# Optimization experiments

Measured on AMD Instinct MI355X. Metric: run time of the kernel, lower is better.

The kernel has to match this reference:

```python
import jax, jax.numpy as jnp
import numpy as np

DIM, N_HEAD, DK, DV = 1024, 16, 64, 64
B, S = 1, 4096


def setup_inputs() -> dict:
    key = jax.random.key(0)
    ks = jax.random.split(key, 9)
    sd = 0.02
    return {
        "x": jax.random.normal(ks[0], (B, S, DIM), dtype=jnp.float32),
        "Wq": jax.random.normal(ks[1], (DIM, N_HEAD * DK), dtype=jnp.float32) * sd,
        "bq": jnp.zeros((N_HEAD * DK,), dtype=jnp.float32),
        "Wk": jax.random.normal(ks[2], (DIM, N_HEAD * DK), dtype=jnp.float32) * sd,
        "bk": jnp.zeros((N_HEAD * DK,), dtype=jnp.float32),
        "Wv": jax.random.normal(ks[3], (DIM, N_HEAD * DV), dtype=jnp.float32) * sd,
        "bv": jnp.zeros((N_HEAD * DV,), dtype=jnp.float32),
        "Wo": jax.random.normal(ks[4], (N_HEAD * DV, DIM), dtype=jnp.float32) * sd,
        "bo": jnp.zeros((DIM,), dtype=jnp.float32),
    }


def reference(x, Wq, bq, Wk, bk, Wv, bv, Wo, bo):
    b, s, _ = x.shape
    scale = DK ** (-0.5)
    # projections -> [b, h, s, d]
    q = (x @ Wq + bq).reshape(b, s, N_HEAD, DK).transpose(0, 2, 1, 3)
    k = (x @ Wk + bk).reshape(b, s, N_HEAD, DK).transpose(0, 2, 1, 3)
    v = (x @ Wv + bv).reshape(b, s, N_HEAD, DV).transpose(0, 2, 1, 3)
    attn = jnp.einsum("bhqd,bhkd->bhqk", q, k) * scale  # [b,h,s,s]
    attn = jax.nn.softmax(attn, axis=-1)
    out = jnp.einsum("bhqk,bhkd->bhqd", attn, v)  # [b,h,s,dv]
    out = out.transpose(0, 2, 1, 3).reshape(b, s, N_HEAD * DV)
    return out @ Wo + bo
```

## Files before the change

kernel.cpp:

```cpp
#include <hip/hip_runtime.h>
#include <hip/hip_bf16.h>
#include <hip/hip_fp16.h>

#define SEQ 4096
#define DIM 1024
#define NH 16

typedef __attribute__((ext_vector_type(4))) float f32x4;
typedef __attribute__((ext_vector_type(8))) _Float16 half8;
typedef __attribute__((ext_vector_type(4))) _Float16 half4;

#if __has_builtin(__builtin_amdgcn_exp2f)
#define EXP2(x) __builtin_amdgcn_exp2f(x)
#else
#define EXP2(x) exp2f(x)
#endif


__global__ __launch_bounds__(256) void conv_x(const float* __restrict__ x,
                                              _Float16* __restrict__ xh, int n) {
  int i = (blockIdx.x * 256 + threadIdx.x) * 4;
  if (i >= n) return;
  float4 v = *reinterpret_cast<const float4*>(x + i);
  half4 h;
  h[0] = (_Float16)v.x; h[1] = (_Float16)v.y;
  h[2] = (_Float16)v.z; h[3] = (_Float16)v.w;
  *reinterpret_cast<half4*>(xh + i) = h;
}

__global__ __launch_bounds__(256) void conv_wT4(const float* __restrict__ W0,
                                                const float* __restrict__ W1,
                                                const float* __restrict__ W2,
                                                const float* __restrict__ W3,
                                                _Float16* __restrict__ T0,
                                                _Float16* __restrict__ T1,
                                                _Float16* __restrict__ T2,
                                                _Float16* __restrict__ T3) {
  const float* W = blockIdx.z == 0 ? W0 : blockIdx.z == 1 ? W1 : blockIdx.z == 2 ? W2 : W3;
  _Float16* Wt = blockIdx.z == 0 ? T0 : blockIdx.z == 1 ? T1 : blockIdx.z == 2 ? T2 : T3;
  __shared__ float t[32][33];
  int bx = blockIdx.x * 32;
  int by = blockIdx.y * 32;
  int tx = threadIdx.x & 31, ty = threadIdx.x >> 5;
#pragma unroll
  for (int i = 0; i < 4; i++)
    t[ty + i * 8][tx] = W[(by + ty + i * 8) * DIM + bx + tx];
  __syncthreads();
#pragma unroll
  for (int i = 0; i < 4; i++)
    Wt[(bx + ty + i * 8) * DIM + by + tx] = (_Float16)t[tx][ty + i * 8];
}

template <int MODE>
__device__ __forceinline__ void gemm_body(const _Float16* __restrict__ A,
                                          const _Float16* __restrict__ Bt,
                                          const float* __restrict__ bias,
                                          void* __restrict__ outp,
                                          int M, int N, int Kd, int bmb, int bnb) {
  __shared__ __align__(16) _Float16 As[64][72];
  __shared__ __align__(16) _Float16 Bs[128][72];
  const int tid = threadIdx.x, lane = tid & 63, w = tid >> 6;
  const int bm = bmb * 64, bn = bnb * 128;
  const int l15 = lane & 15, g = lane >> 4, kb = g * 8;
  const int sra = tid >> 2, sca = (tid & 3) * 16;
  const int srb = tid >> 1, scb = (tid & 1) * 32;
  f32x4 acc[4][2] = {};

  uint4 ar0, ar1, br0, br1, br2, br3;
  auto LOADT = [&](int k0) {
    const _Float16* ap = A + (size_t)(bm + sra) * Kd + k0 + sca;
    ar0 = *reinterpret_cast<const uint4*>(ap);
    ar1 = *reinterpret_cast<const uint4*>(ap + 8);
    const _Float16* bp = Bt + (size_t)(bn + srb) * Kd + k0 + scb;
    br0 = *reinterpret_cast<const uint4*>(bp);
    br1 = *reinterpret_cast<const uint4*>(bp + 8);
    br2 = *reinterpret_cast<const uint4*>(bp + 16);
    br3 = *reinterpret_cast<const uint4*>(bp + 24);
  };

  LOADT(0);
  for (int k0 = 0; k0 < Kd; k0 += 64) {
    __syncthreads();
    *reinterpret_cast<uint4*>(&As[sra][sca]) = ar0;
    *reinterpret_cast<uint4*>(&As[sra][sca + 8]) = ar1;
    *reinterpret_cast<uint4*>(&Bs[srb][scb]) = br0;
    *reinterpret_cast<uint4*>(&Bs[srb][scb + 8]) = br1;
    *reinterpret_cast<uint4*>(&Bs[srb][scb + 16]) = br2;
    *reinterpret_cast<uint4*>(&Bs[srb][scb + 24]) = br3;
    __syncthreads();
    if (k0 + 64 < Kd) LOADT(k0 + 64);
#pragma unroll
    for (int kk = 0; kk < 64; kk += 32) {
      half8 af[4], bf[2];
#pragma unroll
      for (int i = 0; i < 4; i++)
        af[i] = *reinterpret_cast<const half8*>(&As[i * 16 + l15][kk + kb]);
#pragma unroll
      for (int j = 0; j < 2; j++)
        bf[j] = *reinterpret_cast<const half8*>(&Bs[w * 32 + j * 16 + l15][kk + kb]);
      __builtin_amdgcn_s_setprio(1);
#pragma unroll
      for (int i = 0; i < 4; i++)
#pragma unroll
        for (int j = 0; j < 2; j++)
          acc[i][j] = __builtin_amdgcn_mfma_f32_16x16x32_f16(af[i], bf[j], acc[i][j], 0, 0, 0);
      __builtin_amdgcn_s_setprio(0);
    }
  }

#pragma unroll
  for (int i = 0; i < 4; i++)
#pragma unroll
    for (int j = 0; j < 2; j++) {
      const int row0 = bm + i * 16 + g * 4;
      const int col = bn + w * 32 + j * 16 + l15;
      if (MODE == 2) {
        half4 hv;
#pragma unroll
        for (int r = 0; r < 4; r++) hv[r] = (_Float16)(acc[i][j][r] + bias[col]);
        *reinterpret_cast<half4*>(&((_Float16*)outp)[(size_t)col * M + row0]) = hv;
      } else {
#pragma unroll
        for (int r = 0; r < 4; r++) {
          float vv = acc[i][j][r] + bias[col];
          if (MODE == 0) {
            _Float16* O = (_Float16*)outp;
            O[(((col >> 6) * SEQ) + row0 + r) * 64 + (col & 63)] = (_Float16)vv;
          } else {
            float* O = (float*)outp;
            O[(size_t)(row0 + r) * N + col] = vv;
          }
        }
      }
    }
}

__global__ __launch_bounds__(256) void gemm_qkv(const _Float16* __restrict__ A,
                                                const _Float16* __restrict__ WqT,
                                                const _Float16* __restrict__ WkT,
                                                const _Float16* __restrict__ WvT,
                                                const float* __restrict__ bq,
                                                const float* __restrict__ bk,
                                                const float* __restrict__ bv,
                                                _Float16* __restrict__ Qd,
                                                _Float16* __restrict__ Kd,
                                                _Float16* __restrict__ Vd) {
  if (blockIdx.z == 0)
    gemm_body<0>(A, WqT, bq, (void*)Qd, SEQ, DIM, DIM, blockIdx.x, blockIdx.y);
  else if (blockIdx.z == 1)
    gemm_body<0>(A, WkT, bk, (void*)Kd, SEQ, DIM, DIM, blockIdx.x, blockIdx.y);
  else
    gemm_body<2>(A, WvT, bv, (void*)Vd, SEQ, DIM, DIM, blockIdx.x, blockIdx.y);
}

__global__ __launch_bounds__(256) void gemm_out(const _Float16* __restrict__ A,
                                                const _Float16* __restrict__ Bt,
                                                const float* __restrict__ bias,
                                                float* __restrict__ out) {
  gemm_body<1>(A, Bt, bias, (void*)out, SEQ, DIM, DIM, blockIdx.x, blockIdx.y);
}

__global__ __launch_bounds__(256) void attn_fwd(const _Float16* __restrict__ Q,
                                                const _Float16* __restrict__ Kh,
                                                const _Float16* __restrict__ Vt_g,
                                                _Float16* __restrict__ Og) {
  __shared__ __align__(16) _Float16 Ks[64][72];
  __shared__ __align__(16) _Float16 Vs[64][72];
  __shared__ __align__(16) _Float16 Ps[4][2][16][72];
  const int h = blockIdx.y;
  const int q0 = blockIdx.x * 128;
  const int tid = threadIdx.x, lane = tid & 63, w = tid >> 6;
  const int l15 = lane & 15, g = lane >> 4, kb = g * 8;

  const float C = 0.18033688f;

  const int qrow = q0 + w * 32 + l15;
  const _Float16* qp = Q + ((size_t)h * SEQ + qrow) * 64;
  half8 qf[2][2];
  qf[0][0] = *reinterpret_cast<const half8*>(qp + kb);
  qf[0][1] = *reinterpret_cast<const half8*>(qp + 32 + kb);
  qf[1][0] = *reinterpret_cast<const half8*>(qp + 16 * 64 + kb);
  qf[1][1] = *reinterpret_cast<const half8*>(qp + 16 * 64 + 32 + kb);

  f32x4 o[2][4] = {};
  float m[2] = {-1e30f, -1e30f};
  float lsum[2] = {0.f, 0.f};
  float negmC[2] = {1e30f, 1e30f};

  const int srow = tid >> 3, sc8 = (tid & 7) * 8;
  const _Float16* kbase = Kh + (size_t)h * SEQ * 64;
  const _Float16* vbase = Vt_g + (size_t)h * 64 * SEQ;

  uint4 kr0, kr1, vr0, vr1;
  auto LOADKV = [&](int kt2) {
    const _Float16* kp = kbase + (size_t)(kt2 * 64 + srow) * 64 + sc8;
    kr0 = *reinterpret_cast<const uint4*>(kp);
    kr1 = *reinterpret_cast<const uint4*>(kp + 32 * 64);
    const _Float16* vp = vbase + (size_t)srow * SEQ + kt2 * 64 + sc8;
    vr0 = *reinterpret_cast<const uint4*>(vp);
    vr1 = *reinterpret_cast<const uint4*>(vp + 32 * SEQ);
  };

  LOADKV(0);
  for (int kt = 0; kt < SEQ / 64; ++kt) {
    __syncthreads();
    *reinterpret_cast<uint4*>(&Ks[srow][sc8]) = kr0;
    *reinterpret_cast<uint4*>(&Ks[srow + 32][sc8]) = kr1;
    *reinterpret_cast<uint4*>(&Vs[srow][sc8]) = vr0;
    *reinterpret_cast<uint4*>(&Vs[srow + 32][sc8]) = vr1;
    __syncthreads();
    if (kt + 1 < SEQ / 64) LOADKV(kt + 1);

    f32x4 sf[2][4] = {};
    __builtin_amdgcn_s_setprio(1);
#pragma unroll
    for (int f = 0; f < 4; f++) {
      half8 kf0 = *reinterpret_cast<const half8*>(&Ks[f * 16 + l15][kb]);
      half8 kf1 = *reinterpret_cast<const half8*>(&Ks[f * 16 + l15][32 + kb]);
      sf[0][f] = __builtin_amdgcn_mfma_f32_16x16x32_f16(kf0, qf[0][0], sf[0][f], 0, 0, 0);
      sf[0][f] = __builtin_amdgcn_mfma_f32_16x16x32_f16(kf1, qf[0][1], sf[0][f], 0, 0, 0);
      sf[1][f] = __builtin_amdgcn_mfma_f32_16x16x32_f16(kf0, qf[1][0], sf[1][f], 0, 0, 0);
      sf[1][f] = __builtin_amdgcn_mfma_f32_16x16x32_f16(kf1, qf[1][1], sf[1][f], 0, 0, 0);
    }
    __builtin_amdgcn_s_setprio(0);

#pragma unroll
    for (int s = 0; s < 2; s++) {
      float pm = fmaxf(fmaxf(fmaxf(sf[s][0][0], sf[s][0][1]), fmaxf(sf[s][0][2], sf[s][0][3])),
                       fmaxf(fmaxf(sf[s][1][0], sf[s][1][1]), fmaxf(sf[s][1][2], sf[s][1][3])));
      pm = fmaxf(pm, fmaxf(fmaxf(fmaxf(sf[s][2][0], sf[s][2][1]), fmaxf(sf[s][2][2], sf[s][2][3])),
                           fmaxf(fmaxf(sf[s][3][0], sf[s][3][1]), fmaxf(sf[s][3][2], sf[s][3][3]))));
      if (__any(pm > m[s] + 64.f)) {
        pm = fmaxf(pm, __shfl_xor(pm, 16, 64));
        pm = fmaxf(pm, __shfl_xor(pm, 32, 64));
        float mn = fmaxf(m[s], pm);
        float al = EXP2((m[s] - mn) * C);
        m[s] = mn;
        negmC[s] = -mn * C;
        lsum[s] *= al;
#pragma unroll
        for (int f = 0; f < 4; f++) o[s][f] *= al;
      }
      half4 ph[4];
#pragma unroll
      for (int f = 0; f < 4; f++)
#pragma unroll
        for (int r = 0; r < 4; r++) {
          float p = EXP2(fmaf(sf[s][f][r], C, negmC[s]));
          lsum[s] += p;
          ph[f][r] = (_Float16)p;
        }
#pragma unroll
      for (int f = 0; f < 4; f++)
        *reinterpret_cast<half4*>(&Ps[w][s][l15][f * 16 + g * 4]) = ph[f];
    }

    half8 pa[2][2];
#pragma unroll
    for (int s = 0; s < 2; s++) {
      pa[s][0] = *reinterpret_cast<const half8*>(&Ps[w][s][l15][kb]);
      pa[s][1] = *reinterpret_cast<const half8*>(&Ps[w][s][l15][32 + kb]);
    }

    __builtin_amdgcn_s_setprio(1);
#pragma unroll
    for (int f = 0; f < 4; f++) {
      half8 vf0 = *reinterpret_cast<const half8*>(&Vs[f * 16 + l15][kb]);
      half8 vf1 = *reinterpret_cast<const half8*>(&Vs[f * 16 + l15][32 + kb]);
      o[0][f] = __builtin_amdgcn_mfma_f32_16x16x32_f16(vf0, pa[0][0], o[0][f], 0, 0, 0);
      o[0][f] = __builtin_amdgcn_mfma_f32_16x16x32_f16(vf1, pa[0][1], o[0][f], 0, 0, 0);
      o[1][f] = __builtin_amdgcn_mfma_f32_16x16x32_f16(vf0, pa[1][0], o[1][f], 0, 0, 0);
      o[1][f] = __builtin_amdgcn_mfma_f32_16x16x32_f16(vf1, pa[1][1], o[1][f], 0, 0, 0);
    }
    __builtin_amdgcn_s_setprio(0);
  }

#pragma unroll
  for (int s = 0; s < 2; s++) {
    float ls = lsum[s];
    ls += __shfl_xor(ls, 16, 64);
    ls += __shfl_xor(ls, 32, 64);
    float rinv = 1.f / ls;
#pragma unroll
    for (int f = 0; f < 4; f++) {
      half4 hv;
#pragma unroll
      for (int r = 0; r < 4; r++) hv[r] = (_Float16)(o[s][f][r] * rinv);
      *reinterpret_cast<half4*>(
          &Og[(size_t)(qrow + 16 * s) * DIM + h * 64 + f * 16 + g * 4]) = hv;
    }
  }
}


extern "C" void kernel_launch(void* const* d_in, const int* in_sizes, int n_in,
                              void* d_out, int out_size, void* d_ws, size_t ws_size,
                              hipStream_t stream) {
  const float* x  = (const float*)d_in[0];
  const float* Wq = (const float*)d_in[1];
  const float* bq = (const float*)d_in[2];
  const float* Wk = (const float*)d_in[3];
  const float* bk = (const float*)d_in[4];
  const float* Wv = (const float*)d_in[5];
  const float* bv = (const float*)d_in[6];
  const float* Wo = (const float*)d_in[7];
  const float* bo = (const float*)d_in[8];

  char* ws = (char*)d_ws;
  _Float16* xh  = (_Float16*)ws;
  _Float16* WqT = (_Float16*)(ws + (size_t)SEQ * DIM * 2);
  _Float16* WkT = WqT + DIM * DIM;
  _Float16* WvT = WkT + DIM * DIM;
  _Float16* WoT = WvT + DIM * DIM;
  _Float16* Qd  = WoT + DIM * DIM;
  _Float16* Kd  = Qd + (size_t)SEQ * DIM;
  _Float16* Vd  = Kd + (size_t)SEQ * DIM;
  _Float16* Od  = Vd + (size_t)SEQ * DIM;

  conv_x<<<(SEQ * DIM) / 1024, 256, 0, stream>>>(x, xh, SEQ * DIM);
  conv_wT4<<<dim3(32, 32, 4), 256, 0, stream>>>(Wq, Wk, Wv, Wo, WqT, WkT, WvT, WoT);

  gemm_qkv<<<dim3(SEQ / 64, DIM / 128, 3), 256, 0, stream>>>(
      xh, WqT, WkT, WvT, bq, bk, bv, Qd, Kd, Vd);

  attn_fwd<<<dim3(SEQ / 128, NH), 256, 0, stream>>>(Qd, Kd, Vd, Od);

  gemm_out<<<dim3(SEQ / 64, DIM / 128), 256, 0, stream>>>(Od, WoT, bo, (float*)d_out);
}
```

Before: 181.8 us.

## Split attention KV range across two partitions and merge partial softmax results

Splits the key/value sequence of the attention kernel into two partitions along a new grid dimension. Each partition writes unnormalized fp32 partial outputs plus the running max and sum, and a new merge kernel rescales and combines them into the fp16 output. This doubles the number of attention blocks to improve GPU fill and load balance. It costs extra global memory traffic for the fp32 partials, an additional kernel launch, and a larger workspace.

```diff
diff --git a/kernel.cpp b/kernel.cpp
--- a/kernel.cpp
+++ b/kernel.cpp
@@ -5,6 +5,8 @@
 #define SEQ 4096
 #define DIM 1024
 #define NH 16
+#define NSPLIT 2
+#define TILES_PER_PART (SEQ / 64 / NSPLIT)
 
 typedef __attribute__((ext_vector_type(4))) float f32x4;
 typedef __attribute__((ext_vector_type(8))) _Float16 half8;
@@ -15,6 +17,8 @@
 #else
 #define EXP2(x) exp2f(x)
 #endif
+
+#define SMC 0.18033688f
 
 
 __global__ __launch_bounds__(256) void conv_x(const float* __restrict__ x,
@@ -163,16 +167,16 @@
 __global__ __launch_bounds__(256) void attn_fwd(const _Float16* __restrict__ Q,
                                                 const _Float16* __restrict__ Kh,
                                                 const _Float16* __restrict__ Vt_g,
-                                                _Float16* __restrict__ Og) {
+                                                float* __restrict__ Op,
+                                                float2* __restrict__ Ml) {
   __shared__ __align__(16) _Float16 Ks[64][72];
   __shared__ __align__(16) _Float16 Vs[64][72];
   __shared__ __align__(16) _Float16 Ps[4][2][16][72];
   const int h = blockIdx.y;
+  const int part = blockIdx.z;
   const int q0 = blockIdx.x * 128;
   const int tid = threadIdx.x, lane = tid & 63, w = tid >> 6;
   const int l15 = lane & 15, g = lane >> 4, kb = g * 8;
-
-  const float C = 0.18033688f;
 
   const int qrow = q0 + w * 32 + l15;
   const _Float16* qp = Q + ((size_t)h * SEQ + qrow) * 64;
@@ -201,15 +205,16 @@
     vr1 = *reinterpret_cast<const uint4*>(vp + 32 * SEQ);
   };
 
-  LOADKV(0);
-  for (int kt = 0; kt < SEQ / 64; ++kt) {
+  const int t0 = part * TILES_PER_PART, t1 = t0 + TILES_PER_PART;
+  LOADKV(t0);
+  for (int kt = t0; kt < t1; ++kt) {
     __syncthreads();
     *reinterpret_cast<uint4*>(&Ks[srow][sc8]) = kr0;
     *reinterpret_cast<uint4*>(&Ks[srow + 32][sc8]) = kr1;
     *reinterpret_cast<uint4*>(&Vs[srow][sc8]) = vr0;
     *reinterpret_cast<uint4*>(&Vs[srow + 32][sc8]) = vr1;
     __syncthreads();
-    if (kt + 1 < SEQ / 64) LOADKV(kt + 1);
+    if (kt + 1 < t1) LOADKV(kt + 1);
 
     f32x4 sf[2][4] = {};
     __builtin_amdgcn_s_setprio(1);
@@ -234,9 +239,9 @@
         pm = fmaxf(pm, __shfl_xor(pm, 16, 64));
         pm = fmaxf(pm, __shfl_xor(pm, 32, 64));
         float mn = fmaxf(m[s], pm);
-        float al = EXP2((m[s] - mn) * C);
+        float al = EXP2((m[s] - mn) * SMC);
         m[s] = mn;
-        negmC[s] = -mn * C;
+        negmC[s] = -mn * SMC;
         lsum[s] *= al;
 #pragma unroll
         for (int f = 0; f < 4; f++) o[s][f] *= al;
@@ -246,7 +251,7 @@
       for (int f = 0; f < 4; f++)
 #pragma unroll
         for (int r = 0; r < 4; r++) {
-          float p = EXP2(fmaf(sf[s][f][r], C, negmC[s]));
+          float p = EXP2(fmaf(sf[s][f][r], SMC, negmC[s]));
           lsum[s] += p;
           ph[f][r] = (_Float16)p;
         }
@@ -275,21 +280,45 @@
     __builtin_amdgcn_s_setprio(0);
   }
 
+  const size_t prow = ((size_t)part * NH + h) * SEQ;
 #pragma unroll
   for (int s = 0; s < 2; s++) {
     float ls = lsum[s];
     ls += __shfl_xor(ls, 16, 64);
     ls += __shfl_xor(ls, 32, 64);
-    float rinv = 1.f / ls;
+    const size_t rbase = (prow + qrow + 16 * s) * 64;
 #pragma unroll
     for (int f = 0; f < 4; f++) {
-      half4 hv;
-#pragma unroll
-      for (int r = 0; r < 4; r++) hv[r] = (_Float16)(o[s][f][r] * rinv);
-      *reinterpret_cast<half4*>(
-          &Og[(size_t)(qrow + 16 * s) * DIM + h * 64 + f * 16 + g * 4]) = hv;
-    }
+      float4 ov;
+      ov.x = o[s][f][0]; ov.y = o[s][f][1]; ov.z = o[s][f][2]; ov.w = o[s][f][3];
+      *reinterpret_cast<float4*>(&Op[rbase + f * 16 + g * 4]) = ov;
+    }
+    if (g == 0) Ml[prow + qrow + 16 * s] = make_float2(m[s], ls);
   }
+}
+
+__global__ __launch_bounds__(256) void attn_merge(const float* __restrict__ Op,
+                                                  const float2* __restrict__ Ml,
+                                                  _Float16* __restrict__ Og) {
+  const int gid = blockIdx.x * 256 + threadIdx.x;
+  const int dv4 = (gid & 15) * 4;
+  const int row = gid >> 4;
+  const int h = row >> 12, s = row & (SEQ - 1);
+  float2 a = Ml[row];
+  float2 b = Ml[(size_t)NH * SEQ + row];
+  float mm = fmaxf(a.x, b.x);
+  float e1 = EXP2((a.x - mm) * SMC);
+  float e2 = EXP2((b.x - mm) * SMC);
+  float rinv = 1.f / (a.y * e1 + b.y * e2);
+  e1 *= rinv; e2 *= rinv;
+  float4 o1 = *reinterpret_cast<const float4*>(&Op[(size_t)row * 64 + dv4]);
+  float4 o2 = *reinterpret_cast<const float4*>(&Op[((size_t)NH * SEQ + row) * 64 + dv4]);
+  half4 hv;
+  hv[0] = (_Float16)(o1.x * e1 + o2.x * e2);
+  hv[1] = (_Float16)(o1.y * e1 + o2.y * e2);
+  hv[2] = (_Float16)(o1.z * e1 + o2.z * e2);
+  hv[3] = (_Float16)(o1.w * e1 + o2.w * e2);
+  *reinterpret_cast<half4*>(&Og[(size_t)s * DIM + h * 64 + dv4]) = hv;
 }
 
 
@@ -316,6 +345,8 @@
   _Float16* Kd  = Qd + (size_t)SEQ * DIM;
   _Float16* Vd  = Kd + (size_t)SEQ * DIM;
   _Float16* Od  = Vd + (size_t)SEQ * DIM;
+  float*    Opart = (float*)(Od + (size_t)SEQ * DIM);
+  float2*   Mlp   = (float2*)(Opart + (size_t)NSPLIT * NH * SEQ * 64);
 
   conv_x<<<(SEQ * DIM) / 1024, 256, 0, stream>>>(x, xh, SEQ * DIM);
   conv_wT4<<<dim3(32, 32, 4), 256, 0, stream>>>(Wq, Wk, Wv, Wo, WqT, WkT, WvT, WoT);
@@ -323,7 +354,8 @@
   gemm_qkv<<<dim3(SEQ / 64, DIM / 128, 3), 256, 0, stream>>>(
       xh, WqT, WkT, WvT, bq, bk, bv, Qd, Kd, Vd);
 
-  attn_fwd<<<dim3(SEQ / 128, NH), 256, 0, stream>>>(Qd, Kd, Vd, Od);
+  attn_fwd<<<dim3(SEQ / 128, NH, NSPLIT), 256, 0, stream>>>(Qd, Kd, Vd, Opart, Mlp);
+  attn_merge<<<(NH * SEQ * 16) / 256, 256, 0, stream>>>(Opart, Mlp, Od);
 
   gemm_out<<<dim3(SEQ / 64, DIM / 128), 256, 0, stream>>>(Od, WoT, bo, (float*)d_out);
 }
```

New measurement: 195.3 us. 1.07x slower.

## Double-buffer K/V in LDS and feed P to PV MFMA directly from registers

Applied to the files above, without the earlier changes.

The attention kernel now uses two LDS buffers for K and V, so the next tile is staged after compute and each iteration needs one barrier instead of two. It also drops the per-wave P shared-memory round trip. Softmax probabilities are packed with cvt_pkrtz and fed straight into 16x16x16 MFMAs, since that operand layout matches the QK accumulator layout. This removes LDS writes, LDS reads and a barrier per tile, at the cost of twice as many, smaller MFMA instructions, more LDS space, and round-toward-zero conversion of P.

```diff
diff --git a/kernel.cpp b/kernel.cpp
--- a/kernel.cpp
+++ b/kernel.cpp
@@ -5,16 +5,20 @@
 #define SEQ 4096
 #define DIM 1024
 #define NH 16
+#define NT (SEQ / 64)
 
 typedef __attribute__((ext_vector_type(4))) float f32x4;
 typedef __attribute__((ext_vector_type(8))) _Float16 half8;
 typedef __attribute__((ext_vector_type(4))) _Float16 half4;
+typedef __attribute__((ext_vector_type(2))) unsigned uint2v;
 
 #if __has_builtin(__builtin_amdgcn_exp2f)
 #define EXP2(x) __builtin_amdgcn_exp2f(x)
 #else
 #define EXP2(x) exp2f(x)
 #endif
+
+#define SMC 0.18033688f
 
 
 __global__ __launch_bounds__(256) void conv_x(const float* __restrict__ x,
@@ -164,15 +168,12 @@
                                                 const _Float16* __restrict__ Kh,
                                                 const _Float16* __restrict__ Vt_g,
                                                 _Float16* __restrict__ Og) {
-  __shared__ __align__(16) _Float16 Ks[64][72];
-  __shared__ __align__(16) _Float16 Vs[64][72];
-  __shared__ __align__(16) _Float16 Ps[4][2][16][72];
+  __shared__ __align__(16) _Float16 Ks[2][64][72];
+  __shared__ __align__(16) _Float16 Vs[2][64][72];
   const int h = blockIdx.y;
   const int q0 = blockIdx.x * 128;
   const int tid = threadIdx.x, lane = tid & 63, w = tid >> 6;
   const int l15 = lane & 15, g = lane >> 4, kb = g * 8;
-
-  const float C = 0.18033688f;
 
   const int qrow = q0 + w * 32 + l15;
   const _Float16* qp = Q + ((size_t)h * SEQ + qrow) * 64;
@@ -200,23 +201,28 @@
     vr0 = *reinterpret_cast<const uint4*>(vp);
     vr1 = *reinterpret_cast<const uint4*>(vp + 32 * SEQ);
   };
+  auto STAGE = [&](int buf) {
+    *reinterpret_cast<uint4*>(&Ks[buf][srow][sc8]) = kr0;
+    *reinterpret_cast<uint4*>(&Ks[buf][srow + 32][sc8]) = kr1;
+    *reinterpret_cast<uint4*>(&Vs[buf][srow][sc8]) = vr0;
+    *reinterpret_cast<uint4*>(&Vs[buf][srow + 32][sc8]) = vr1;
+  };
 
   LOADKV(0);
-  for (int kt = 0; kt < SEQ / 64; ++kt) {
-    __syncthreads();
-    *reinterpret_cast<uint4*>(&Ks[srow][sc8]) = kr0;
-    *reinterpret_cast<uint4*>(&Ks[srow + 32][sc8]) = kr1;
-    *reinterpret_cast<uint4*>(&Vs[srow][sc8]) = vr0;
-    *reinterpret_cast<uint4*>(&Vs[srow + 32][sc8]) = vr1;
-    __syncthreads();
-    if (kt + 1 < SEQ / 64) LOADKV(kt + 1);
+  STAGE(0);
+  __syncthreads();
+  int cur = 0;
+
+  for (int kt = 0; kt < NT; ++kt) {
+    const bool more = (kt + 1 < NT);
+    if (more) LOADKV(kt + 1);
 
     f32x4 sf[2][4] = {};
     __builtin_amdgcn_s_setprio(1);
 #pragma unroll
     for (int f = 0; f < 4; f++) {
-      half8 kf0 = *reinterpret_cast<const half8*>(&Ks[f * 16 + l15][kb]);
-      half8 kf1 = *reinterpret_cast<const half8*>(&Ks[f * 16 + l15][32 + kb]);
+      half8 kf0 = *reinterpret_cast<const half8*>(&Ks[cur][f * 16 + l15][kb]);
+      half8 kf1 = *reinterpret_cast<const half8*>(&Ks[cur][f * 16 + l15][32 + kb]);
       sf[0][f] = __builtin_amdgcn_mfma_f32_16x16x32_f16(kf0, qf[0][0], sf[0][f], 0, 0, 0);
       sf[0][f] = __builtin_amdgcn_mfma_f32_16x16x32_f16(kf1, qf[0][1], sf[0][f], 0, 0, 0);
       sf[1][f] = __builtin_amdgcn_mfma_f32_16x16x32_f16(kf0, qf[1][0], sf[1][f], 0, 0, 0);
@@ -224,6 +230,7 @@
     }
     __builtin_amdgcn_s_setprio(0);
 
+    half4 pb[2][4];
 #pragma unroll
     for (int s = 0; s < 2; s++) {
       float pm = fmaxf(fmaxf(fmaxf(sf[s][0][0], sf[s][0][1]), fmaxf(sf[s][0][2], sf[s][0][3])),
@@ -234,45 +241,42 @@
         pm = fmaxf(pm, __shfl_xor(pm, 16, 64));
         pm = fmaxf(pm, __shfl_xor(pm, 32, 64));
         float mn = fmaxf(m[s], pm);
-        float al = EXP2((m[s] - mn) * C);
+        float al = EXP2((m[s] - mn) * SMC);
         m[s] = mn;
-        negmC[s] = -mn * C;
+        negmC[s] = -mn * SMC;
         lsum[s] *= al;
 #pragma unroll
         for (int f = 0; f < 4; f++) o[s][f] *= al;
       }
-      half4 ph[4];
-#pragma unroll
-      for (int f = 0; f < 4; f++)
-#pragma unroll
-        for (int r = 0; r < 4; r++) {
-          float p = EXP2(fmaf(sf[s][f][r], C, negmC[s]));
-          lsum[s] += p;
-          ph[f][r] = (_Float16)p;
-        }
-#pragma unroll
-      for (int f = 0; f < 4; f++)
-        *reinterpret_cast<half4*>(&Ps[w][s][l15][f * 16 + g * 4]) = ph[f];
-    }
-
-    half8 pa[2][2];
-#pragma unroll
-    for (int s = 0; s < 2; s++) {
-      pa[s][0] = *reinterpret_cast<const half8*>(&Ps[w][s][l15][kb]);
-      pa[s][1] = *reinterpret_cast<const half8*>(&Ps[w][s][l15][32 + kb]);
+#pragma unroll
+      for (int f = 0; f < 4; f++) {
+        float p0 = EXP2(fmaf(sf[s][f][0], SMC, negmC[s]));
+        float p1 = EXP2(fmaf(sf[s][f][1], SMC, negmC[s]));
+        float p2 = EXP2(fmaf(sf[s][f][2], SMC, negmC[s]));
+        float p3 = EXP2(fmaf(sf[s][f][3], SMC, negmC[s]));
+        lsum[s] += (p0 + p1) + (p2 + p3);
+        auto h01 = __builtin_amdgcn_cvt_pkrtz(p0, p1);
+        auto h23 = __builtin_amdgcn_cvt_pkrtz(p2, p3);
+        uint2v uu = {__builtin_bit_cast(unsigned, h01), __builtin_bit_cast(unsigned, h23)};
+        pb[s][f] = __builtin_bit_cast(half4, uu);
+      }
     }
 
     __builtin_amdgcn_s_setprio(1);
 #pragma unroll
-    for (int f = 0; f < 4; f++) {
-      half8 vf0 = *reinterpret_cast<const half8*>(&Vs[f * 16 + l15][kb]);
-      half8 vf1 = *reinterpret_cast<const half8*>(&Vs[f * 16 + l15][32 + kb]);
-      o[0][f] = __builtin_amdgcn_mfma_f32_16x16x32_f16(vf0, pa[0][0], o[0][f], 0, 0, 0);
-      o[0][f] = __builtin_amdgcn_mfma_f32_16x16x32_f16(vf1, pa[0][1], o[0][f], 0, 0, 0);
-      o[1][f] = __builtin_amdgcn_mfma_f32_16x16x32_f16(vf0, pa[1][0], o[1][f], 0, 0, 0);
-      o[1][f] = __builtin_amdgcn_mfma_f32_16x16x32_f16(vf1, pa[1][1], o[1][f], 0, 0, 0);
+    for (int fv = 0; fv < 4; fv++) {
+#pragma unroll
+      for (int fk = 0; fk < 4; fk++) {
+        half4 va = *reinterpret_cast<const half4*>(&Vs[cur][fv * 16 + l15][fk * 16 + g * 4]);
+        o[0][fv] = __builtin_amdgcn_mfma_f32_16x16x16f16(va, pb[0][fk], o[0][fv], 0, 0, 0);
+        o[1][fv] = __builtin_amdgcn_mfma_f32_16x16x16f16(va, pb[1][fk], o[1][fv], 0, 0, 0);
+      }
     }
     __builtin_amdgcn_s_setprio(0);
+
+    if (more) STAGE(cur ^ 1);
+    __syncthreads();
+    cur ^= 1;
   }
 
 #pragma unroll
```

Measured after the change: 188.6 us. 1.04x slower.
